# Kernel tuning notes

Hardware: AMD Instinct MI355X
Metric: run time of the kernel (lower is better)

Reference implementation:

```python
import jax, jax.numpy as jnp
import numpy as np
from jax import lax

EPS = 1e-20  # matches sample_gumbel eps in the TF source


def setup_inputs() -> dict:
    key = jax.random.key(0)
    ks = jax.random.split(key, 7)
    B, T, D, H, K = 32, 512, 512, 512, 64
    x = jax.random.normal(ks[0], (B, T, D), jnp.float32)
    f_after = jax.random.normal(ks[1], (K, D, H), jnp.float32) * 0.02
    f_skip = jax.random.normal(ks[2], (2 * H, 2), jnp.float32) * 0.05
    gru_kernel = jax.random.normal(ks[3], (D, 3 * H), jnp.float32) * 0.02
    gru_rec_kernel = jax.random.normal(ks[4], (H, 3 * H), jnp.float32) * 0.02
    gru_bias = jnp.zeros((2, 3 * H), jnp.float32)
    u_gumbel = jax.random.uniform(ks[5], (T, B, 2), jnp.float32)
    return {"x": x, "f_after": f_after, "f_skip": f_skip,
            "gru_kernel": gru_kernel, "gru_rec_kernel": gru_rec_kernel,
            "gru_bias": gru_bias, "u_gumbel": u_gumbel}


def reference(x, f_after, f_skip, gru_kernel, gru_rec_kernel, gru_bias, u_gumbel):
    # z_after = tanh(conv1d(x, f_after, SAME))  -> [B, T, H]
    z_after = lax.conv_general_dilated(
        x, f_after, window_strides=(1,), padding='SAME',
        dimension_numbers=('NWC', 'WIO', 'NWC'))
    z_after = jnp.tanh(z_after)

    # gumbel(0,1) noise from uniform draws, per step: [T, B, 2]
    g = -jnp.log(-jnp.log(u_gumbel + EPS) + EPS)

    b_in, b_rec = gru_bias[0], gru_bias[1]  # reset_after=True biases, each [3H]
    H = gru_rec_kernel.shape[0]
    B = x.shape[0]
    h0 = jnp.zeros((B, H), x.dtype)

    xs = (jnp.swapaxes(x, 0, 1), jnp.swapaxes(z_after, 0, 1), g)  # time-major

    def step(h_prev, inp):
        x_t, za_t, g_t = inp
        # skip gate: concat(h_{t-1}, z_after_t) @ f_skip, gumbel-softmax (temp=1)
        logits = jnp.concatenate([h_prev, za_t], axis=-1) @ f_skip  # [B, 2]
        skip = jax.nn.softmax(logits + g_t, axis=-1)
        # Keras GRUCell (reset_after=True), gate order z, r, h
        xm = x_t @ gru_kernel + b_in          # [B, 3H]
        hm = h_prev @ gru_rec_kernel + b_rec  # [B, 3H]
        xz, xr, xh = jnp.split(xm, 3, axis=-1)
        hz, hr, hh = jnp.split(hm, 3, axis=-1)
        z = jax.nn.sigmoid(xz + hz)
        r = jax.nn.sigmoid(xr + hr)
        hc = jnp.tanh(xh + r * hh)
        ht = z * h_prev + (1.0 - z) * hc
        # skip blend
        ht = skip[:, 0:1] * h_prev + skip[:, 1:2] * ht
        return ht, ht

    _, ys = lax.scan(step, h0, xs)           # [T, B, H]
    return jnp.swapaxes(ys, 0, 1)            # [B, T, H]
```

## Files before the change

### kernel.cpp

```cpp
#include <hip/hip_runtime.h>
#include <stdint.h>

typedef unsigned short u16;
typedef unsigned int   u32;
typedef __attribute__((ext_vector_type(8))) short short8;
typedef __attribute__((ext_vector_type(4))) float f32x4;
typedef __attribute__((ext_vector_type(4))) u32   u32x4;

#define AS1 __attribute__((address_space(1)))
#define AS3 __attribute__((address_space(3)))

#define SENT 0x7FC0u
#define HS   528

__device__ __forceinline__ float bf2f(u16 u) {
  union { u32 i; float f; } v; v.i = ((u32)u) << 16; return v.f;
}
__device__ __forceinline__ u16 f2bf(float f) {
  union { float f; u32 i; } v; v.f = f;
  u32 i = v.i;
  i += 0x7FFFu + ((i >> 16) & 1u);
  return (u16)(i >> 16);
}
__device__ __forceinline__ float tanh_fast(float x) {
  const float e = __expf(-2.f * fabsf(x));
  const float t = (1.f - e) / (1.f + e);
  return __builtin_copysignf(t, x);
}

__device__ __forceinline__ void gload16(const u16* src, u16* ldsDst) {
  __builtin_amdgcn_global_load_lds((const AS1 u32*)src, (AS3 u32*)ldsDst, 16, 0, 0);
}

__device__ __forceinline__ short8 ldg_sc_h_wait(const u16* p) {
  short8 r;
  asm volatile("global_load_dwordx4 %0, %1, off sc0 sc1\n\t"
               "s_waitcnt vmcnt(0)"
               : "=v"(r) : "v"(p) : "memory");
  return r;
}
__device__ __forceinline__ void stg_sc_h(u16* p, u16 v) {
  asm volatile("global_store_short %0, %1, off sc0 sc1" :: "v"(p), "v"((u32)v) : "memory");
}

__global__ void k_init(const float* __restrict__ x, u16* __restrict__ xp) {
  const long NXP = 32L * 576 * 512;
  long i0 = (long)blockIdx.x * 256 + threadIdx.x;
  for (long i = i0; i < NXP; i += (long)gridDim.x * 256) {
    long b = i / (576 * 512);
    int rem = (int)(i - b * (576 * 512));
    int rr = rem >> 9, dd = rem & 511;
    int t = rr - 31;
    float v = (t >= 0 && t < 512) ? x[(b * 512 + t) * 512 + dd] : 0.f;
    xp[i] = f2bf(v);
  }
}

__global__ void k_sent(u32* __restrict__ hs) {
  const u32x4 s = u32x4{(SENT << 16) | SENT, (SENT << 16) | SENT,
                        (SENT << 16) | SENT, (SENT << 16) | SENT};
  *(u32x4*)&hs[((long)blockIdx.x * 256 + threadIdx.x) * 4] = s;
}

__global__ void k_transpose_cast(const float* __restrict__ in, u16* __restrict__ out,
                                 int rows, int cols, long inWStride, long outWStride) {
  __shared__ float tile[64][65];
  const int w = blockIdx.z;
  const float* ip = in + (long)w * inWStride;
  u16* op = out + (long)w * outWStride;
  const int r0 = blockIdx.y * 64, c0 = blockIdx.x * 64;
  const int tr = threadIdx.x >> 6, tc = threadIdx.x & 63;
  #pragma unroll
  for (int p = 0; p < 16; ++p) {
    int rr = p * 4 + tr;
    tile[rr][tc] = ip[(long)(r0 + rr) * cols + c0 + tc];
  }
  __syncthreads();
  #pragma unroll
  for (int p = 0; p < 16; ++p) {
    int rr = p * 4 + tr;
    op[(long)(c0 + rr) * rows + r0 + tc] = f2bf(tile[tc][rr]);
  }
}

__global__ __launch_bounds__(256, 1) void k_conv(
    const u16* __restrict__ A, const u16* __restrict__ Bm, u16* __restrict__ C)
{
  __shared__ __align__(16) u16 Abig[2][320 * 64];
  __shared__ __align__(16) u16 Blds[3][128 * 64];
  const int bid0 = blockIdx.x;
  const int bid = (bid0 & 7) * 32 + (bid0 >> 3);
  const int mt = bid & 63, nt = bid >> 6;
  const int h0 = nt * 128;
  const int b = mt >> 1;
  const int t0 = (mt & 1) * 256;
  const long row0 = (long)mt * 256;
  const int tid = threadIdx.x;
  const int wv = tid >> 6, l = tid & 63;
  const int wr = wv >> 1, wc = wv & 1;
  const int sRow = wv * 8 + (l >> 3);
  const int sColSw = ((l & 7) ^ (l >> 3)) * 8;
  f32x4 acc[8][4];
  #pragma unroll
  for (int m = 0; m < 8; ++m)
    #pragma unroll
    for (int n = 0; n < 4; ++n) acc[m][n] = f32x4{0.f, 0.f, 0.f, 0.f};

  const long aRow0 = (long)b * 576 + t0;

  auto stageA = [&](int d) {
    const int dcol = d << 6;
    #pragma unroll
    for (int c = 0; c < 10; ++c)
      gload16(A + (aRow0 + c * 32 + sRow) * 512 + dcol + sColSw,
              &Abig[d & 1][(c * 32 + wv * 8) * 64]);
  };
  auto stageB = [&](int p) {
    const int d = p >> 6, w = p & 63;
    const u16* bB = Bm + ((long)w << 18) + (long)h0 * 512 + (d << 6) + sColSw;
    #pragma unroll
    for (int c = 0; c < 4; ++c)
      gload16(bB + (long)(c * 32 + sRow) * 512, &Blds[p % 3][(c * 32 + wv * 8) * 64]);
  };

  stageA(0); stageB(0); stageB(1);
  for (int p = 0; p < 512; ++p) {
    const int d = p >> 6, w = p & 63;
    if (p + 2 < 512) stageB(p + 2);
    if (w == 0 && d < 7) stageA(d + 1);
    if (p >= 510)              asm volatile("s_waitcnt vmcnt(0)"  ::: "memory");
    else if (w <= 2 && d < 7)  asm volatile("s_waitcnt vmcnt(18)" ::: "memory");
    else                       asm volatile("s_waitcnt vmcnt(8)"  ::: "memory");
    __builtin_amdgcn_s_barrier();
    __builtin_amdgcn_sched_barrier(0);
    const u16* Ab = &Abig[d & 1][0];
    const u16* Bb = &Blds[p % 3][0];
    #pragma unroll
    for (int kk = 0; kk < 2; ++kk) {
      short8 af[8], bf[4];
      #pragma unroll
      for (int m = 0; m < 8; ++m) {
        const int row = w + wr * 128 + m * 16 + (l & 15);
        const int ci = (kk * 32 + (l >> 4) * 8) ^ ((row & 7) * 8);
        af[m] = *(const short8*)&Ab[row * 64 + ci];
      }
      #pragma unroll
      for (int n = 0; n < 4; ++n) {
        const int row = wc * 64 + n * 16 + (l & 15);
        const int ci = (kk * 32 + (l >> 4) * 8) ^ ((row & 7) * 8);
        bf[n] = *(const short8*)&Bb[row * 64 + ci];
      }
      #pragma unroll
      for (int m = 0; m < 8; ++m)
        #pragma unroll
        for (int n = 0; n < 4; ++n)
          acc[m][n] = __builtin_amdgcn_mfma_f32_16x16x32_bf16(af[m], bf[n], acc[m][n], 0, 0, 0);
    }
    __builtin_amdgcn_s_barrier();
  }
  const int lr = (l >> 4) * 4, lc = l & 15;
  #pragma unroll
  for (int m = 0; m < 8; ++m)
    #pragma unroll
    for (int n = 0; n < 4; ++n)
      #pragma unroll
      for (int r = 0; r < 4; ++r) {
        const long row = row0 + wr * 128 + m * 16 + lr + r;
        const int col = h0 + wc * 64 + n * 16 + lc;
        C[row * 512 + col] = f2bf(tanhf(acc[m][n][r]));
      }
}

__global__ __launch_bounds__(256) void k_gemm(
    const u16* __restrict__ A, const u16* __restrict__ Bm, u16* __restrict__ C,
    int nTiles, int kw, int woff, long bWStride, int outMode)
{
  __shared__ __align__(16) u16 Alds[128 * 64];
  __shared__ __align__(16) u16 Blds[128 * 64];
  const int bid0 = blockIdx.x;
  const int cpx = gridDim.x >> 3;
  const int bid = (bid0 & 7) * cpx + (bid0 >> 3);
  const int mt = bid / nTiles, nt = bid - mt * nTiles;
  const int bb = (mt * 128) >> 9;
  const int t0 = (mt * 128) & 511;
  const int h0 = nt * 128;
  const int tid = threadIdx.x;
  const int wv = tid >> 6, l = tid & 63;
  const int wr = wv >> 1, wc = wv & 1;
  const int sRow = wv * 8 + (l >> 3);
  const int sCol = (l & 7) * 8;
  f32x4 acc[4][4];
  #pragma unroll
  for (int m = 0; m < 4; ++m)
    #pragma unroll
    for (int n = 0; n < 4; ++n) acc[m][n] = f32x4{0.f, 0.f, 0.f, 0.f};

  const int kIters = kw * 8;
  const long aRow0 = (long)(bb * 576 + t0 + woff);
  for (int q = 0; q < kIters; ++q) {
    const int w = q >> 3, dsub = (q & 7) << 6;
    const u16* aB = A + (aRow0 + w) * 512 + dsub + sCol;
    const u16* bB = Bm + (long)w * bWStride + (long)h0 * 512 + dsub + sCol;
    __syncthreads();
    #pragma unroll
    for (int c = 0; c < 4; ++c) {
      gload16(aB + (long)(c * 32 + sRow) * 512, &Alds[c * 2048 + wv * 512]);
      gload16(bB + (long)(c * 32 + sRow) * 512, &Blds[c * 2048 + wv * 512]);
    }
    __syncthreads();
    #pragma unroll
    for (int kk = 0; kk < 2; ++kk) {
      short8 af[4], bf[4];
      #pragma unroll
      for (int m = 0; m < 4; ++m)
        af[m] = *(const short8*)&Alds[(wr * 64 + m * 16 + (l & 15)) * 64 + kk * 32 + (l >> 4) * 8];
      #pragma unroll
      for (int n = 0; n < 4; ++n)
        bf[n] = *(const short8*)&Blds[(wc * 64 + n * 16 + (l & 15)) * 64 + kk * 32 + (l >> 4) * 8];
      #pragma unroll
      for (int m = 0; m < 4; ++m)
        #pragma unroll
        for (int n = 0; n < 4; ++n)
          acc[m][n] = __builtin_amdgcn_mfma_f32_16x16x32_bf16(af[m], bf[n], acc[m][n], 0, 0, 0);
    }
  }
  const int lr = (l >> 4) * 4, lc = l & 15;
  #pragma unroll
  for (int m = 0; m < 4; ++m)
    #pragma unroll
    for (int n = 0; n < 4; ++n)
      #pragma unroll
      for (int r = 0; r < 4; ++r) {
        const int row = mt * 128 + wr * 64 + m * 16 + lr + r;
        const int col = h0 + wc * 64 + n * 16 + lc;
        const float v = acc[m][n][r];
        if (outMode == 0) {
          C[(long)row * 512 + col] = f2bf(tanhf(v));
        } else {
          const int b = row >> 9, t = row & 511;
          C[((long)t * 32 + b) * 1536 + col] = f2bf(v);
        }
      }
}

__global__ void k_dza(const u16* __restrict__ za, const float* __restrict__ fskip,
                      const float* __restrict__ ug, float* __restrict__ dza) {
  __shared__ float wd2[512];
  const int t = blockIdx.x, tid = threadIdx.x;
  for (int i = tid; i < 512; i += 256) wd2[i] = fskip[(512 + i) * 2 + 1] - fskip[(512 + i) * 2];
  __syncthreads();
  const int b = tid >> 3, seg = (tid & 7) * 64;
  const u16* row = za + ((long)b * 512 + t) * 512 + seg;
  float pp = 0.f;
  #pragma unroll
  for (int j = 0; j < 8; ++j) {
    short8 v = *(const short8*)&row[j * 8];
    #pragma unroll
    for (int e = 0; e < 8; ++e) pp += bf2f((u16)v[e]) * wd2[seg + j * 8 + e];
  }
  pp += __shfl_xor(pp, 1); pp += __shfl_xor(pp, 2); pp += __shfl_xor(pp, 4);
  if ((tid & 7) == 0) {
    float u0 = ug[((long)t * 32 + b) * 2 + 0], u1 = ug[((long)t * 32 + b) * 2 + 1];
    float g0 = -logf(-logf(u0 + 1e-20f) + 1e-20f);
    float g1 = -logf(-logf(u1 + 1e-20f) + 1e-20f);
    dza[t * 32 + b] = pp + (g1 - g0);
  }
}

__global__ __launch_bounds__(256, 1) void k_rnn(
    const u16* __restrict__ XM, const float* __restrict__ dza,
    const float* __restrict__ Wrec, const float* __restrict__ gbias,
    const float* __restrict__ fskip, u16* hstep, float* __restrict__ out)
{
  const int bid = blockIdx.x, d = bid & 7, s = bid >> 3;
  const int tid = threadIdx.x, wv = tid >> 6, l = tid & 63;
  __shared__ __align__(16) u16 hBl[2][4 * HS];
  __shared__ float s1s[2][4];

  float wdv[8];
  #pragma unroll
  for (int e = 0; e < 8; ++e)
    wdv[e] = fskip[(l * 8 + e) * 2 + 1] - fskip[(l * 8 + e) * 2];

  const int colb = s * 64 + wv * 16 + (l & 15);
  const int kq = (l >> 4) * 8;

  short8 wf[3][16];
  #pragma unroll
  for (int g = 0; g < 3; ++g)
    #pragma unroll
    for (int kk = 0; kk < 16; ++kk) {
      short8 tmp;
      #pragma unroll
      for (int e = 0; e < 8; ++e)
        tmp[e] = (short)f2bf(Wrec[(long)(kk * 32 + kq + e) * 1536 + g * 512 + colb]);
      wf[g][kk] = tmp;
    }
  float bi[3], br[3];
  #pragma unroll
  for (int g = 0; g < 3; ++g) {
    bi[g] = gbias[g * 512 + colb];
    br[g] = gbias[1536 + g * 512 + colb];
  }
  const int myb = d * 4;
  float hp[4] = {0.f, 0.f, 0.f, 0.f};
  float hnv[4] = {0.f, 0.f, 0.f, 0.f};

  u16 xmc[3][4];
  float dzc;
  if (l < 16) {
    const u16* xr = XM + (long)myb * 1536;
    #pragma unroll
    for (int r = 0; r < 4; ++r)
      #pragma unroll
      for (int g = 0; g < 3; ++g)
        xmc[g][r] = xr[(long)r * 1536 + g * 512 + colb];
  }
  dzc = dza[myb + wv];

  for (int t = 0; t < 512; ++t) {
    const int p = t & 1;

    short8 h8;
    if (t > 0) {
      const u16* ph = hstep + ((long)(t - 1) * 32 + myb + wv) * 512 + l * 8;
      h8 = ldg_sc_h_wait(ph);
      bool bad = true;
      while (bad) {
        bad = false;
        #pragma unroll
        for (int e = 0; e < 8; ++e) bad |= ((u16)h8[e] == SENT);
        if (bad) h8 = ldg_sc_h_wait(ph);
      }
    } else {
      #pragma unroll
      for (int e = 0; e < 8; ++e) h8[e] = 0;
    }

    if (t > 0 && l < 16) {
      #pragma unroll
      for (int r = 0; r < 4; ++r)
        out[((long)(myb + r) * 512 + (t - 1)) * 512 + colb] = hnv[r];
    }

    u16 xmn[3][4];
    const int tn = (t < 511) ? t + 1 : t;
    if (l < 16) {
      const u16* xr = XM + ((long)tn * 32 + myb) * 1536;
      #pragma unroll
      for (int r = 0; r < 4; ++r)
        #pragma unroll
        for (int g = 0; g < 3; ++g)
          xmn[g][r] = xr[(long)r * 1536 + g * 512 + colb];
    }
    const float dzn = dza[tn * 32 + myb + wv];

    *(short8*)&hBl[p][wv * HS + l * 8] = h8;
    float pp = 0.f;
    #pragma unroll
    for (int e = 0; e < 8; ++e) pp += bf2f((u16)h8[e]) * wdv[e];
    #pragma unroll
    for (int o = 1; o < 64; o <<= 1) pp += __shfl_xor(pp, o);
    if (l == 0) s1s[p][wv] = 1.f / (1.f + __expf(-(pp + dzc)));
    __syncthreads();

    f32x4 acc[3];
    acc[0] = f32x4{0.f, 0.f, 0.f, 0.f}; acc[1] = acc[0]; acc[2] = acc[0];
    const int b4 = l & 3;
    #pragma unroll
    for (int kk = 0; kk < 16; ++kk) {
      short8 a = *(const short8*)&hBl[p][b4 * HS + kk * 32 + kq];
      acc[0] = __builtin_amdgcn_mfma_f32_16x16x32_bf16(a, wf[0][kk], acc[0], 0, 0, 0);
      acc[1] = __builtin_amdgcn_mfma_f32_16x16x32_bf16(a, wf[1][kk], acc[1], 0, 0, 0);
      acc[2] = __builtin_amdgcn_mfma_f32_16x16x32_bf16(a, wf[2][kk], acc[2], 0, 0, 0);
    }

    if (l < 16) {
      #pragma unroll
      for (int r = 0; r < 4; ++r) {
        const float xz = bf2f(xmc[0][r]) + bi[0];
        const float xr_ = bf2f(xmc[1][r]) + bi[1];
        const float xh = bf2f(xmc[2][r]) + bi[2];
        const float hz = acc[0][r] + br[0];
        const float hr = acc[1][r] + br[1];
        const float hh = acc[2][r] + br[2];
        const float z  = 1.f / (1.f + __expf(-(xz + hz)));
        const float rr = 1.f / (1.f + __expf(-(xr_ + hr)));
        const float hc = tanh_fast(xh + rr * hh);
        const float ht = z * hp[r] + (1.f - z) * hc;
        const float s1 = s1s[p][r];
        const float hn = hp[r] + s1 * (ht - hp[r]);
        stg_sc_h(&hstep[((long)t * 32 + myb + r) * 512 + colb], f2bf(hn));
        hp[r] = hn;
        hnv[r] = hn;
      }
      #pragma unroll
      for (int g = 0; g < 3; ++g)
        #pragma unroll
        for (int r = 0; r < 4; ++r) xmc[g][r] = xmn[g][r];
    }
    dzc = dzn;
  }
  if (l < 16) {
    #pragma unroll
    for (int r = 0; r < 4; ++r)
      out[((long)(myb + r) * 512 + 511) * 512 + colb] = hnv[r];
  }
}

extern "C" void kernel_launch(void* const* d_in, const int* in_sizes, int n_in,
                              void* d_out, int out_size, void* d_ws, size_t ws_size,
                              hipStream_t stream) {
  (void)in_sizes; (void)n_in; (void)out_size; (void)ws_size;
  const float* x        = (const float*)d_in[0];
  const float* f_after  = (const float*)d_in[1];
  const float* f_skip   = (const float*)d_in[2];
  const float* gru_k    = (const float*)d_in[3];
  const float* gru_rec  = (const float*)d_in[4];
  const float* gru_bias = (const float*)d_in[5];
  const float* ug       = (const float*)d_in[6];
  float* out = (float*)d_out;

  char* ws = (char*)d_ws;
  size_t off = 0;
  auto alloc = [&](size_t bytes) { void* p = ws + off; off = (off + bytes + 255) & ~(size_t)255; return p; };
  u16*  xp    = (u16*)alloc(32L * 576 * 512 * 2);
  u16*  fT    = (u16*)alloc(64L * 512 * 512 * 2);
  u16*  gruT  = (u16*)alloc(1536L * 512 * 2);
  u16*  za    = (u16*)alloc(32L * 512 * 512 * 2);
  u16*  XM    = (u16*)alloc(512L * 32 * 1536 * 2);
  float* dza  = (float*)alloc(512L * 32 * 4);
  u16*  hstep = za;

  k_init<<<dim3(4096), dim3(256), 0, stream>>>(x, xp);
  k_transpose_cast<<<dim3(8, 8, 64), dim3(256), 0, stream>>>(f_after, fT, 512, 512, 512L * 512, 512L * 512);
  k_transpose_cast<<<dim3(24, 8, 1), dim3(256), 0, stream>>>(gru_k, gruT, 512, 1536, 0L, 0L);
  k_conv<<<dim3(256), dim3(256), 0, stream>>>(xp, fT, za);
  k_gemm<<<dim3(1536), dim3(256), 0, stream>>>(xp, gruT, XM, 12, 1, 31, 0L, 1);
  k_dza<<<dim3(512), dim3(256), 0, stream>>>(za, f_skip, ug, dza);
  k_sent<<<dim3(4096), dim3(256), 0, stream>>>((u32*)hstep);
  k_rnn<<<dim3(64), dim3(256), 0, stream>>>(XM, dza, gru_rec, gru_bias, f_skip, hstep, out);
}
```

Measured before the change: 1.952 ms.

## Prefetch next-step hidden state early and serve own slice from LDS

After: 2.217 ms. 1.14x slower.

```diff
diff --git a/kernel.cpp b/kernel.cpp
--- a/kernel.cpp
+++ b/kernel.cpp
@@ -275,6 +275,7 @@
   const int bid = blockIdx.x, d = bid & 7, s = bid >> 3;
   const int tid = threadIdx.x, wv = tid >> 6, l = tid & 63;
   __shared__ __align__(16) u16 hBl[2][4 * HS];
+  __shared__ __align__(16) u16 hOwn[2][4][64];
   __shared__ float s1s[2][4];
 
   float wdv[8];
@@ -318,19 +319,32 @@
   }
   dzc = dza[myb + wv];
 
+  short8 h8pre;
+  #pragma unroll
+  for (int e = 0; e < 8; ++e) h8pre[e] = 0;
+
   for (int t = 0; t < 512; ++t) {
     const int p = t & 1;
 
     short8 h8;
     if (t > 0) {
-      const u16* ph = hstep + ((long)(t - 1) * 32 + myb + wv) * 512 + l * 8;
-      h8 = ldg_sc_h_wait(ph);
-      bool bad = true;
+      asm volatile("s_waitcnt vmcnt(4) lgkmcnt(0)" ::: "memory");
+      __builtin_amdgcn_sched_barrier(0);
+      __builtin_amdgcn_s_barrier();
+      __builtin_amdgcn_sched_barrier(0);
+      h8 = h8pre;
+      if ((l >> 3) == s)
+        h8 = *(const short8*)&hOwn[p ^ 1][wv][(l & 7) * 8];
+      bool bad = false;
+      #pragma unroll
+      for (int e = 0; e < 8; ++e) bad |= ((u16)h8[e] == SENT);
       while (bad) {
+        const u16* ph = hstep + ((long)(t - 1) * 32 + myb + wv) * 512 + l * 8;
+        short8 hr = ldg_sc_h_wait(ph);
+        if ((l >> 3) != s) h8 = hr;
         bad = false;
         #pragma unroll
         for (int e = 0; e < 8; ++e) bad |= ((u16)h8[e] == SENT);
-        if (bad) h8 = ldg_sc_h_wait(ph);
       }
     } else {
       #pragma unroll
@@ -362,7 +376,10 @@
     #pragma unroll
     for (int o = 1; o < 64; o <<= 1) pp += __shfl_xor(pp, o);
     if (l == 0) s1s[p][wv] = 1.f / (1.f + __expf(-(pp + dzc)));
-    __syncthreads();
+    asm volatile("s_waitcnt lgkmcnt(0)" ::: "memory");
+    __builtin_amdgcn_sched_barrier(0);
+    __builtin_amdgcn_s_barrier();
+    __builtin_amdgcn_sched_barrier(0);
 
     f32x4 acc[3];
     acc[0] = f32x4{0.f, 0.f, 0.f, 0.f}; acc[1] = acc[0]; acc[2] = acc[0];
@@ -375,6 +392,7 @@
       acc[2] = __builtin_amdgcn_mfma_f32_16x16x32_bf16(a, wf[2][kk], acc[2], 0, 0, 0);
     }
 
+    u16 hb4[4];
     if (l < 16) {
       #pragma unroll
       for (int r = 0; r < 4; ++r) {
@@ -390,9 +408,10 @@
         const float ht = z * hp[r] + (1.f - z) * hc;
         const float s1 = s1s[p][r];
         const float hn = hp[r] + s1 * (ht - hp[r]);
-        stg_sc_h(&hstep[((long)t * 32 + myb + r) * 512 + colb], f2bf(hn));
         hp[r] = hn;
         hnv[r] = hn;
+        hb4[r] = f2bf(hn);
+        hOwn[p][r][wv * 16 + l] = hb4[r];
       }
       #pragma unroll
       for (int g = 0; g < 3; ++g)
@@ -400,6 +419,18 @@
         for (int r = 0; r < 4; ++r) xmc[g][r] = xmn[g][r];
     }
     dzc = dzn;
+
+    __builtin_amdgcn_sched_barrier(0);
+    {
+      const u16* ph = hstep + ((long)t * 32 + myb + wv) * 512 + l * 8;
+      asm volatile("global_load_dwordx4 %0, %1, off sc0 sc1"
+                   : "=v"(h8pre) : "v"(ph) : "memory");
+    }
+    if (l < 16) {
+      #pragma unroll
+      for (int r = 0; r < 4; ++r)
+        stg_sc_h(&hstep[((long)t * 32 + myb + r) * 512 + colb], hb4[r]);
+    }
   }
   if (l < 16) {
     #pragma unroll
```
